# Kernel optimization log

Hardware: AMD Instinct MI355X
Metric: run time of the kernel (lower is better)

Reference implementation:

```python
import jax, jax.numpy as jnp
import numpy as np

B, P, CD, RD, H, NR, OD, T = 1024, 22, 256, 64, 512, 12, 2, 100
IN = OD + 2 + CD + RD  # 324: [pos(2), ball(2), context(256), role_embed(64)]


def setup_inputs() -> dict:
    key = jax.random.key(0)
    ks = jax.random.split(key, 20)
    def n(k, shape, s=1.0):
        return jax.random.normal(k, shape, dtype=jnp.float32) * s
    sH = 1.0 / np.sqrt(H)
    sI = 1.0 / np.sqrt(IN)
    return {
        "context": n(ks[0], (B, P, CD)),
        "initial_position": n(ks[1], (B, P, OD)),
        "ball_landing": n(ks[2], (B, 2)),
        "roles": jax.random.randint(ks[3], (B, P), 0, NR, dtype=jnp.int32),
        "max_steps": T,
        "role_table": n(ks[4], (NR, RD), 0.02),
        # LSTM layer 0 (input_dim=IN)
        "W_ih0": n(ks[5], (4 * H, IN), sI),
        "W_hh0": n(ks[6], (4 * H, H), sH),
        "b0": n(ks[7], (4 * H,), sH),  # b_ih + b_hh fused
        # LSTM layer 1 (input_dim=H)
        "W_ih1": n(ks[8], (4 * H, H), sH),
        "W_hh1": n(ks[9], (4 * H, H), sH),
        "b1": n(ks[10], (4 * H,), sH),
        # output MLP: H -> H//2 -> OD
        "W_fc1": n(ks[11], (H // 2, H), sH),
        "b_fc1": n(ks[12], (H // 2,), sH),
        "W_fc2": n(ks[13], (OD, H // 2), 1.0 / np.sqrt(H // 2)),
        "b_fc2": n(ks[14], (OD,), 0.02),
        # initial_pos_encoder: Linear(OD, H)
        "W_init": n(ks[15], (H, OD), 1.0 / np.sqrt(OD)),
        "b_init": n(ks[16], (H,), 0.02),
    }


def _lstm_cell(x, h, c, W_ih, W_hh, b):
    # PyTorch gate order: i, f, g, o
    gates = x @ W_ih.T + h @ W_hh.T + b  # [N, 4H]
    i, f, g, o = jnp.split(gates, 4, axis=-1)
    c_new = jax.nn.sigmoid(f) * c + jax.nn.sigmoid(i) * jnp.tanh(g)
    h_new = jax.nn.sigmoid(o) * jnp.tanh(c_new)
    return h_new, c_new


def reference(context, initial_position, ball_landing, roles, max_steps,
              role_table, W_ih0, W_hh0, b0, W_ih1, W_hh1, b1,
              W_fc1, b_fc1, W_fc2, b_fc2, W_init, b_init):
    batch, num_players, context_dim = context.shape
    N = batch * num_players
    out_dim = initial_position.shape[-1]

    ctx_flat = context.reshape(N, context_dim)
    role_flat = role_table[roles].reshape(N, -1)
    ball_flat = jnp.broadcast_to(ball_landing[:, None, :], (batch, num_players, 2)).reshape(N, 2)
    static = jnp.concatenate([ball_flat, ctx_flat, role_flat], axis=1)  # [N, IN-2]

    pos0 = initial_position.reshape(N, out_dim)
    h0 = pos0 @ W_init.T + b_init  # initial_pos_encoder into layer-0 hidden
    c0 = jnp.zeros_like(h0)
    h1 = jnp.zeros_like(h0)
    c1 = jnp.zeros_like(h0)

    def step(carry, _):
        pos, h0, c0, h1, c1 = carry
        x = jnp.concatenate([pos, static], axis=1)  # [N, IN]
        h0, c0 = _lstm_cell(x, h0, c0, W_ih0, W_hh0, b0)
        h1, c1 = _lstm_cell(h0, h1, c1, W_ih1, W_hh1, b1)
        # output MLP (dropout inactive in eval)
        nxt = jax.nn.relu(h1 @ W_fc1.T + b_fc1) @ W_fc2.T + b_fc2  # [N, OD]
        return (nxt, h0, c0, h1, c1), nxt

    _, preds = jax.lax.scan(step, (pos0, h0, c0, h1, c1), None, length=max_steps)
    # preds: [T, N, OD] -> [batch, num_players, T, OD]
    preds = preds.transpose(1, 0, 2).reshape(batch, num_players, max_steps, out_dim)
    return preds
```

## Files before the change

### kernel.cpp

```cpp
#include <hip/hip_runtime.h>
#include <cstdint>


#define DEVI __device__ __forceinline__

typedef __bf16 bf16x8 __attribute__((ext_vector_type(8)));
typedef float  f32x4  __attribute__((ext_vector_type(4)));
typedef float  f32x2  __attribute__((ext_vector_type(2)));
typedef unsigned short u16x4 __attribute__((ext_vector_type(4)));

static constexpr int NROWS = 22528;
static constexpr int T_STEPS = 100;
static constexpr int NBM = 176;

DEVI unsigned short f2bf(float f) {
  unsigned u = __float_as_uint(f);
  u = u + 0x7FFFu + ((u >> 16) & 1u);
  return (unsigned short)(u >> 16);
}
DEVI float bf2f(unsigned short h) { return __uint_as_float(((unsigned)h) << 16); }

DEVI float fast_sigmoid(float x) {
  float e = __builtin_amdgcn_exp2f(-1.442695041f * x);
  return __builtin_amdgcn_rcpf(1.0f + e);
}
DEVI float fast_tanh(float x) {
  float e = __builtin_amdgcn_exp2f(2.885390082f * x);
  return 1.0f - 2.0f * __builtin_amdgcn_rcpf(e + 1.0f);
}

DEVI void async_copy16(const void* g, void* l) {
  __builtin_amdgcn_global_load_lds(
      (const __attribute__((address_space(1))) void*)g,
      (__attribute__((address_space(3))) void*)l, 16, 0, 0);
}

template <int KITERS, int KSWITCH>
DEVI void gemm_core(const unsigned short* __restrict__ A1, int lda1,
                    const unsigned short* __restrict__ A2, int lda2,
                    const unsigned short* __restrict__ B1, int ldb1,
                    const unsigned short* __restrict__ B2, int ldb2,
                    unsigned short* lds, f32x4 acc[4][4], int tid) {
  const int lane = tid & 63, wid = tid >> 6;
  const int wm = wid & 1, wn = wid >> 1;
  const int c16 = lane & 15, q = lane >> 4;
#pragma unroll
  for (int i = 0; i < 4; ++i)
#pragma unroll
    for (int j = 0; j < 4; ++j) acc[i][j] = f32x4{0.f, 0.f, 0.f, 0.f};
#pragma unroll
  for (int kt = 0; kt < KITERS; ++kt) {
    const bool sec = (kt >= KSWITCH);
    const unsigned short* Ab = sec ? A2 : A1;
    const unsigned short* Bb = sec ? B2 : B1;
    const int lda = sec ? lda2 : lda1;
    const int ldb = sec ? ldb2 : ldb1;
    const int kk = (sec ? (kt - KSWITCH) : kt) * 64;
    __syncthreads();
#pragma unroll
    for (int rd = 0; rd < 4; ++rd) {
      int p = rd * 256 + tid;
      int row = p >> 3, u = p & 7, ch = u ^ (row & 7);
      async_copy16(Ab + row * lda + kk + ch * 8, lds + p * 8);
      async_copy16(Bb + row * ldb + kk + ch * 8, lds + 8192 + p * 8);
    }
    __syncthreads();
#pragma unroll
    for (int s = 0; s < 2; ++s) {
      bf16x8 a[4], b[4];
#pragma unroll
      for (int mf = 0; mf < 4; ++mf) {
        int row = wm * 64 + mf * 16 + c16;
        int slot = row * 8 + ((s * 4 + q) ^ (row & 7));
        a[mf] = *(const bf16x8*)(lds + slot * 8);
      }
#pragma unroll
      for (int nf = 0; nf < 4; ++nf) {
        int row = wn * 64 + nf * 16 + c16;
        int slot = row * 8 + ((s * 4 + q) ^ (row & 7));
        b[nf] = *(const bf16x8*)(lds + 8192 + slot * 8);
      }
#pragma unroll
      for (int mf = 0; mf < 4; ++mf)
#pragma unroll
        for (int nf = 0; nf < 4; ++nf)
          acc[mf][nf] = __builtin_amdgcn_mfma_f32_16x16x32_bf16(a[mf], b[nf], acc[mf][nf], 0, 0, 0);
    }
  }
}

DEVI int orig_row(int j) {
  int tile = j >> 7, rem = j & 127;
  int half = rem >> 6, g = (rem >> 4) & 3, cc = rem & 15;
  return g * 512 + (tile * 32 + half * 16 + cc);
}

__global__ void k_prep_w(const float* __restrict__ Whh0, const float* __restrict__ Wih1,
                         const float* __restrict__ Whh1, const float* __restrict__ Wih0,
                         const float* __restrict__ Wfc1, const float* __restrict__ b0,
                         const float* __restrict__ b1,
                         unsigned short* __restrict__ W0p, unsigned short* __restrict__ Wc1p,
                         unsigned short* __restrict__ Wsp, unsigned short* __restrict__ Wfc1b,
                         float* __restrict__ Wposx, float* __restrict__ Wposy,
                         float* __restrict__ b0p4, float* __restrict__ b1p4) {
  int j = blockIdx.x;
  int k = threadIdx.x;
  int o = orig_row(j);
  W0p[j * 512 + k]         = f2bf(Whh0[o * 512 + k]);
  Wc1p[j * 1024 + k]       = f2bf(Wih1[o * 512 + k]);
  Wc1p[j * 1024 + 512 + k] = f2bf(Whh1[o * 512 + k]);
  if (k < 384) Wsp[j * 384 + k] = (k < 322) ? f2bf(Wih0[o * 324 + 2 + k]) : (unsigned short)0;
  if (k == 0) {
    int g = (j >> 4) & 3;
    int cg = (j >> 7) * 32 + ((j >> 6) & 1) * 16 + (j & 15);
    Wposx[cg * 4 + g] = Wih0[o * 324 + 0];
    Wposy[cg * 4 + g] = Wih0[o * 324 + 1];
    b0p4[cg * 4 + g] = b0[o];
    b1p4[cg * 4 + g] = b1[o];
  }
  if (j < 256) Wfc1b[j * 512 + k] = f2bf(Wfc1[j * 512 + k]);
}

__global__ void k_init_xs(const float* __restrict__ ball, const float* __restrict__ ctx,
                          const int* __restrict__ roles, const float* __restrict__ role_table,
                          unsigned short* __restrict__ Xs) {
  int n = blockIdx.x, col = threadIdx.x;
  int b = n / 22;
  float v;
  if (col < 2)        v = ball[b * 2 + col];
  else if (col < 258) v = ctx[(size_t)n * 256 + col - 2];
  else if (col < 322) v = role_table[roles[n] * 64 + col - 258];
  else                v = 0.f;
  Xs[(size_t)n * 384 + col] = f2bf(v);
}

__global__ void k_init_state(const float* __restrict__ pos0, const float* __restrict__ Winit,
                             const float* __restrict__ binit, unsigned short* __restrict__ Hcat,
                             float* __restrict__ c0, float* __restrict__ c1,
                             float* __restrict__ posb) {
  int idx = blockIdx.x * 256 + threadIdx.x;
  if (idx >= NROWS * 512) return;
  int n = idx >> 9, c = idx & 511;
  float px = pos0[n * 2 + 0], py = pos0[n * 2 + 1];
  float h0 = binit[c] + Winit[c * 2 + 0] * px + Winit[c * 2 + 1] * py;
  Hcat[(size_t)n * 1024 + c] = f2bf(h0);
  Hcat[(size_t)n * 1024 + 512 + c] = 0;
  c0[idx] = 0.f;
  c1[idx] = 0.f;
  if (c < 2) posb[n * 2 + c] = pos0[n * 2 + c];
}

__global__ __launch_bounds__(256) void k_static(const unsigned short* __restrict__ Xs,
                                                const unsigned short* __restrict__ Wsp,
                                                const float* __restrict__ b0p4,
                                                unsigned short* __restrict__ SP2) {
  __shared__ __align__(16) unsigned short lds[16384];
  int tid = threadIdx.x, bn = blockIdx.x, bm = blockIdx.y;
  f32x4 acc[4][4];
  const unsigned short* Ab = Xs + (size_t)bm * 128 * 384;
  const unsigned short* Bb = Wsp + (size_t)bn * 128 * 384;
  gemm_core<6, 6>(Ab, 384, Ab, 384, Bb, 384, Bb, 384, lds, acc, tid);
  int lane = tid & 63, wid = tid >> 6, wm = wid & 1, wn = wid >> 1;
  int c16 = lane & 15, q = lane >> 4;
  int cg = bn * 32 + wn * 16 + c16;
  f32x4 bb = *(const f32x4*)&b0p4[cg * 4];
#pragma unroll
  for (int mf = 0; mf < 4; ++mf) {
    int row0 = bm * 128 + wm * 64 + mf * 16 + q * 4;
#pragma unroll
    for (int r = 0; r < 4; ++r) {
      u16x4 v;
      v.x = f2bf(acc[mf][0][r] + bb.x);
      v.y = f2bf(acc[mf][1][r] + bb.y);
      v.z = f2bf(acc[mf][2][r] + bb.z);
      v.w = f2bf(acc[mf][3][r] + bb.w);
      ((u16x4*)SP2)[(size_t)(row0 + r) * 512 + cg] = v;
    }
  }
}

DEVI void swz(int l, int& bn, int& bm) {
  int xcd = l & 7, i = l >> 3;
  bn = i & 15;
  bm = xcd + 8 * (i >> 4);
}

template <bool USE_SP>
__global__ __launch_bounds__(256) void k_s1(const unsigned short* __restrict__ cur,
                                            const unsigned short* __restrict__ Xs,
                                            const unsigned short* __restrict__ W0p,
                                            const unsigned short* __restrict__ Wsp,
                                            const unsigned short* __restrict__ SP2,
                                            const float* __restrict__ b0p4,
                                            const float* __restrict__ Wposx,
                                            const float* __restrict__ Wposy,
                                            const float* __restrict__ posb,
                                            float* __restrict__ c0,
                                            unsigned short* __restrict__ nxt) {
  __shared__ __align__(16) unsigned short lds[16384];
  int tid = threadIdx.x, bn, bm;
  swz(blockIdx.x, bn, bm);
  f32x4 acc[4][4];
  const unsigned short* A1 = cur + (size_t)bm * 128 * 1024;
  const unsigned short* B1 = W0p + (size_t)bn * 128 * 512;
  if constexpr (USE_SP) {
    gemm_core<8, 8>(A1, 1024, A1, 1024, B1, 512, B1, 512, lds, acc, tid);
  } else {
    const unsigned short* A2 = Xs + (size_t)bm * 128 * 384;
    const unsigned short* B2 = Wsp + (size_t)bn * 128 * 384;
    gemm_core<14, 8>(A1, 1024, A2, 384, B1, 512, B2, 384, lds, acc, tid);
  }
  int lane = tid & 63, wid = tid >> 6, wm = wid & 1, wn = wid >> 1;
  int c16 = lane & 15, q = lane >> 4;
  int cg = bn * 32 + wn * 16 + c16;
  f32x4 wpx = *(const f32x4*)&Wposx[cg * 4];
  f32x4 wpy = *(const f32x4*)&Wposy[cg * 4];
  f32x4 sb = f32x4{0.f, 0.f, 0.f, 0.f};
  if constexpr (!USE_SP) sb = *(const f32x4*)&b0p4[cg * 4];
#pragma unroll
  for (int mf = 0; mf < 4; ++mf) {
    int row0 = bm * 128 + wm * 64 + mf * 16 + q * 4;
    f32x4 cold = *(const f32x4*)&c0[(size_t)cg * NROWS + row0];
    f32x4 cnew;
#pragma unroll
    for (int r = 0; r < 4; ++r) {
      size_t row = row0 + r;
      f32x2 pv = *(const f32x2*)&posb[row * 2];
      float s0 = sb.x, s1 = sb.y, s2 = sb.z, s3 = sb.w;
      if constexpr (USE_SP) {
        u16x4 sp = ((const u16x4*)SP2)[row * 512 + cg];
        s0 = bf2f(sp.x); s1 = bf2f(sp.y); s2 = bf2f(sp.z); s3 = bf2f(sp.w);
      }
      float gi = acc[mf][0][r] + s0 + pv.x * wpx.x + pv.y * wpy.x;
      float gf = acc[mf][1][r] + s1 + pv.x * wpx.y + pv.y * wpy.y;
      float gg = acc[mf][2][r] + s2 + pv.x * wpx.z + pv.y * wpy.z;
      float go = acc[mf][3][r] + s3 + pv.x * wpx.w + pv.y * wpy.w;
      float cn = fast_sigmoid(gf) * cold[r] + fast_sigmoid(gi) * fast_tanh(gg);
      cnew[r] = cn;
      nxt[row * 1024 + cg] = f2bf(fast_sigmoid(go) * fast_tanh(cn));
    }
    *(f32x4*)&c0[(size_t)cg * NROWS + row0] = cnew;
  }
}

__global__ __launch_bounds__(256) void k_s2(const unsigned short* __restrict__ nxt_in,
                                            const unsigned short* __restrict__ cur,
                                            const unsigned short* __restrict__ Wc1p,
                                            const float* __restrict__ b1p4,
                                            float* __restrict__ c1,
                                            unsigned short* __restrict__ nxt_out) {
  __shared__ __align__(16) unsigned short lds[16384];
  int tid = threadIdx.x, bn, bm;
  swz(blockIdx.x, bn, bm);
  f32x4 acc[4][4];
  const unsigned short* A1 = nxt_in + (size_t)bm * 128 * 1024;
  const unsigned short* A2 = cur + (size_t)bm * 128 * 1024 + 512;
  const unsigned short* B1 = Wc1p + (size_t)bn * 128 * 1024;
  gemm_core<16, 8>(A1, 1024, A2, 1024, B1, 1024, B1 + 512, 1024, lds, acc, tid);
  int lane = tid & 63, wid = tid >> 6, wm = wid & 1, wn = wid >> 1;
  int c16 = lane & 15, q = lane >> 4;
  int cg = bn * 32 + wn * 16 + c16;
  f32x4 bv = *(const f32x4*)&b1p4[cg * 4];
#pragma unroll
  for (int mf = 0; mf < 4; ++mf) {
    int row0 = bm * 128 + wm * 64 + mf * 16 + q * 4;
    f32x4 cold = *(const f32x4*)&c1[(size_t)cg * NROWS + row0];
    f32x4 cnew;
#pragma unroll
    for (int r = 0; r < 4; ++r) {
      size_t row = row0 + r;
      float gi = acc[mf][0][r] + bv.x;
      float gf = acc[mf][1][r] + bv.y;
      float gg = acc[mf][2][r] + bv.z;
      float go = acc[mf][3][r] + bv.w;
      float cn = fast_sigmoid(gf) * cold[r] + fast_sigmoid(gi) * fast_tanh(gg);
      cnew[r] = cn;
      nxt_out[row * 1024 + 512 + cg] = f2bf(fast_sigmoid(go) * fast_tanh(cn));
    }
    *(f32x4*)&c1[(size_t)cg * NROWS + row0] = cnew;
  }
}

__global__ __launch_bounds__(256) void k_s3(const unsigned short* __restrict__ H,
                                            const unsigned short* __restrict__ Wfc1b,
                                            const float* __restrict__ bfc1,
                                            const float* __restrict__ Wfc2,
                                            const float* __restrict__ bfc2,
                                            float* __restrict__ out, float* __restrict__ posb,
                                            int t) {
  __shared__ __align__(16) unsigned short ldsA[32 * 64];
  __shared__ __align__(16) unsigned short ldsB[256 * 64];
  __shared__ float wfc2s[512];
  __shared__ float red[32 * 8];
  int tid = threadIdx.x;
  int l = blockIdx.x, xcd = l & 7, i = l >> 3;
  int b32 = 4 * (xcd + 8 * (i >> 2)) + (i & 3);
  wfc2s[tid] = Wfc2[tid];
  wfc2s[tid + 256] = Wfc2[tid + 256];
  int lane = tid & 63, wid = tid >> 6;
  int c16 = lane & 15, q = lane >> 4;
  f32x4 acc[2][4];
#pragma unroll
  for (int ii = 0; ii < 2; ++ii)
#pragma unroll
    for (int jj = 0; jj < 4; ++jj) acc[ii][jj] = f32x4{0.f, 0.f, 0.f, 0.f};
  const unsigned short* Ab = H + (size_t)b32 * 32 * 1024 + 512;
#pragma unroll
  for (int kt = 0; kt < 8; ++kt) {
    int k0 = kt * 64;
    __syncthreads();
    {
      int p = tid;
      int row = p >> 3, u = p & 7, ch = u ^ (row & 7);
      async_copy16(Ab + row * 1024 + k0 + ch * 8, ldsA + p * 8);
    }
#pragma unroll
    for (int rd = 0; rd < 8; ++rd) {
      int p = rd * 256 + tid;
      int row = p >> 3, u = p & 7, ch = u ^ (row & 7);
      async_copy16(Wfc1b + row * 512 + k0 + ch * 8, ldsB + p * 8);
    }
    __syncthreads();
#pragma unroll
    for (int s = 0; s < 2; ++s) {
      bf16x8 a[2], b[4];
#pragma unroll
      for (int mf = 0; mf < 2; ++mf) {
        int row = mf * 16 + c16;
        int slot = row * 8 + ((s * 4 + q) ^ (row & 7));
        a[mf] = *(const bf16x8*)(ldsA + slot * 8);
      }
#pragma unroll
      for (int nf = 0; nf < 4; ++nf) {
        int row = wid * 64 + nf * 16 + c16;
        int slot = row * 8 + ((s * 4 + q) ^ (row & 7));
        b[nf] = *(const bf16x8*)(ldsB + slot * 8);
      }
#pragma unroll
      for (int mf = 0; mf < 2; ++mf)
#pragma unroll
        for (int nf = 0; nf < 4; ++nf)
          acc[mf][nf] = __builtin_amdgcn_mfma_f32_16x16x32_bf16(a[mf], b[nf], acc[mf][nf], 0, 0, 0);
    }
  }
  float part[2][2][4];
#pragma unroll
  for (int d = 0; d < 2; ++d)
#pragma unroll
    for (int mf = 0; mf < 2; ++mf)
#pragma unroll
      for (int r = 0; r < 4; ++r) part[d][mf][r] = 0.f;
#pragma unroll
  for (int nf = 0; nf < 4; ++nf) {
    int col = wid * 64 + nf * 16 + c16;
    float w0 = wfc2s[col], w1 = wfc2s[256 + col], bv = bfc1[col];
#pragma unroll
    for (int mf = 0; mf < 2; ++mf)
#pragma unroll
      for (int r = 0; r < 4; ++r) {
        float v = acc[mf][nf][r] + bv;
        v = v > 0.f ? v : 0.f;
        part[0][mf][r] += v * w0;
        part[1][mf][r] += v * w1;
      }
  }
#pragma unroll
  for (int st = 1; st < 16; st <<= 1)
#pragma unroll
    for (int d = 0; d < 2; ++d)
#pragma unroll
      for (int mf = 0; mf < 2; ++mf)
#pragma unroll
        for (int r = 0; r < 4; ++r)
          part[d][mf][r] += __shfl_xor(part[d][mf][r], st, 64);
  if (c16 == 0) {
#pragma unroll
    for (int mf = 0; mf < 2; ++mf)
#pragma unroll
      for (int r = 0; r < 4; ++r) {
        int rl = mf * 16 + q * 4 + r;
        red[rl * 8 + wid * 2 + 0] = part[0][mf][r];
        red[rl * 8 + wid * 2 + 1] = part[1][mf][r];
      }
  }
  __syncthreads();
  if (tid < 64) {
    int rl = tid >> 1, d = tid & 1;
    float s = red[rl * 8 + d] + red[rl * 8 + 2 + d] + red[rl * 8 + 4 + d]
            + red[rl * 8 + 6 + d] + bfc2[d];
    int rg = b32 * 32 + rl;
    out[((size_t)rg * T_STEPS + t) * 2 + d] = s;
    posb[rg * 2 + d] = s;
  }
}

extern "C" void kernel_launch(void* const* d_in, const int* in_sizes, int n_in,
                              void* d_out, int out_size, void* d_ws, size_t ws_size,
                              hipStream_t stream) {
  (void)in_sizes; (void)n_in; (void)out_size;
  const float* ctx   = (const float*)d_in[0];
  const float* pos0  = (const float*)d_in[1];
  const float* ball  = (const float*)d_in[2];
  const int*   roles = (const int*)d_in[3];
  const float* role_table = (const float*)d_in[5];
  const float* Wih0 = (const float*)d_in[6];
  const float* Whh0 = (const float*)d_in[7];
  const float* b0   = (const float*)d_in[8];
  const float* Wih1 = (const float*)d_in[9];
  const float* Whh1 = (const float*)d_in[10];
  const float* b1   = (const float*)d_in[11];
  const float* Wfc1 = (const float*)d_in[12];
  const float* bfc1 = (const float*)d_in[13];
  const float* Wfc2 = (const float*)d_in[14];
  const float* bfc2 = (const float*)d_in[15];
  const float* Winit = (const float*)d_in[16];
  const float* binit = (const float*)d_in[17];
  float* out = (float*)d_out;

  char* w = (char*)d_ws;
  size_t used = 0;
  auto alloc = [&](size_t bytes) {
    char* p = w + used;
    used += (bytes + 255) & ~(size_t)255;
    return p;
  };
  unsigned short* W0p   = (unsigned short*)alloc((size_t)2048 * 512 * 2);
  unsigned short* Wc1p  = (unsigned short*)alloc((size_t)2048 * 1024 * 2);
  unsigned short* Wfc1b = (unsigned short*)alloc((size_t)256 * 512 * 2);
  float* Wposx = (float*)alloc(2048 * 4);
  float* Wposy = (float*)alloc(2048 * 4);
  float* b0p4  = (float*)alloc(2048 * 4);
  float* b1p4  = (float*)alloc(2048 * 4);
  float* posb  = (float*)alloc((size_t)NROWS * 2 * 4);
  unsigned short* Hc0 = (unsigned short*)alloc((size_t)NROWS * 1024 * 2);
  float* c0   = (float*)alloc((size_t)NROWS * 512 * 4);
  float* c1   = (float*)alloc((size_t)NROWS * 512 * 4);
  unsigned short* Hc1 = (unsigned short*)alloc((size_t)NROWS * 1024 * 2);

  const size_t SP_BYTES = (size_t)NROWS * 2048 * 2;
  const bool use_sp = (ws_size >= used + SP_BYTES + (1u << 20));

  unsigned short *Xs, *Wsp, *SP2;
  if (use_sp) {
    SP2 = (unsigned short*)alloc(SP_BYTES);
    Xs  = Hc1;
    Wsp = Hc1 + (size_t)NROWS * 384;
  } else {
    SP2 = Hc1;
    Xs  = (unsigned short*)alloc((size_t)NROWS * 384 * 2);
    Wsp = (unsigned short*)alloc((size_t)2048 * 384 * 2);
  }

  k_prep_w<<<2048, 512, 0, stream>>>(Whh0, Wih1, Whh1, Wih0, Wfc1, b0, b1,
                                     W0p, Wc1p, Wsp, Wfc1b, Wposx, Wposy, b0p4, b1p4);
  k_init_xs<<<NROWS, 384, 0, stream>>>(ball, ctx, roles, role_table, Xs);
  k_init_state<<<(NROWS * 512 + 255) / 256, 256, 0, stream>>>(pos0, Winit, binit, Hc0, c0, c1, posb);

  if (use_sp) {
    dim3 gs(16, NBM);
    k_static<<<gs, 256, 0, stream>>>(Xs, Wsp, b0p4, SP2);
  }

  for (int t = 0; t < T_STEPS; ++t) {
    unsigned short* cur = (t & 1) ? Hc1 : Hc0;
    unsigned short* nxt = (t & 1) ? Hc0 : Hc1;
    if (use_sp)
      k_s1<true><<<16 * NBM, 256, 0, stream>>>(cur, Xs, W0p, Wsp, SP2, b0p4, Wposx, Wposy, posb, c0, nxt);
    else
      k_s1<false><<<16 * NBM, 256, 0, stream>>>(cur, Xs, W0p, Wsp, SP2, b0p4, Wposx, Wposy, posb, c0, nxt);
    k_s2<<<16 * NBM, 256, 0, stream>>>(nxt, cur, Wc1p, b1p4, c1, nxt);
    k_s3<<<704, 256, 0, stream>>>(nxt, Wfc1b, bfc1, Wfc2, bfc2, out, posb, t);
  }
}
```

Measured before the change: 22.08 ms.

## Use 256x256 tiles with 8-wave pipelined double-buffered GEMM for LSTM steps

Replaces the 128x128, 4-wave GEMM core in both per-step LSTM kernels with a 256x256 tile, 512-thread kernel. The new kernel uses a deeper asynchronous LDS staging pipeline over four half-K buffers and raises MFMA priority with setprio. The larger tiles halve global and LDS traffic per output and overlap loads with MFMA work. In exchange, each block uses 128KB of LDS and more registers for 8x4 accumulators, and the grid shrinks to 704 blocks, which may limit occupancy and wave balance across CUs.

```diff
diff --git a/kernel.cpp b/kernel.cpp
--- a/kernel.cpp
+++ b/kernel.cpp
@@ -179,47 +179,163 @@
   }
 }
 
-DEVI void swz(int l, int& bn, int& bm) {
-  int xcd = l & 7, i = l >> 3;
-  bn = i & 15;
-  bm = xcd + 8 * (i >> 4);
+
+struct GemmSrc {
+  const unsigned short *A1, *A2, *B1, *B2;
+  int ldA1, ldA2, ldB1, ldB2;
+};
+
+template <int KT, int KSW>
+DEVI void stage_q(const GemmSrc& g, int t, int s, int isB, unsigned short* dst, int tid) {
+  int tt = (t >= KT) ? (t - 2) : t;
+  const bool sec = (tt >= KSW);
+  const unsigned short* base;
+  int ld;
+  if (isB) { base = sec ? g.B2 : g.B1; ld = sec ? g.ldB2 : g.ldB1; }
+  else     { base = sec ? g.A2 : g.A1; ld = sec ? g.ldA2 : g.ldA1; }
+  base += (sec ? (tt - KSW) : tt) * 64 + s * 32;
+#pragma unroll
+  for (int rd = 0; rd < 2; ++rd) {
+    int p = rd * 512 + tid;
+    int row = p >> 2, u = p & 3, ch = u ^ ((row >> 1) & 3);
+    async_copy16(base + row * ld + ch * 8, dst + p * 8);
+  }
+}
+
+#define GBAR   asm volatile("s_barrier" ::: "memory")
+#define VMCNT4 asm volatile("s_waitcnt vmcnt(4)" ::: "memory")
+
+template <int KT, int KSW>
+DEVI void gemm8(const GemmSrc& g, unsigned short* lds, f32x4 acc[8][4], int tid) {
+  const int lane = tid & 63, wid = tid >> 6;
+  const int wm = wid >> 2, wn = wid & 3;
+  const int c16 = lane & 15, q = lane >> 4;
+#pragma unroll
+  for (int i = 0; i < 8; ++i)
+#pragma unroll
+    for (int j = 0; j < 4; ++j) acc[i][j] = f32x4{0.f, 0.f, 0.f, 0.f};
+  unsigned short* A00 = lds;
+  unsigned short* A01 = lds + 8192;
+  unsigned short* B00 = lds + 16384;
+  unsigned short* B01 = lds + 24576;
+  unsigned short* A10 = lds + 32768;
+  unsigned short* A11 = lds + 40960;
+  unsigned short* B10 = lds + 49152;
+  unsigned short* B11 = lds + 57344;
+  const int rowA0 = wm * 128 + c16;
+  const int rowB0 = wn * 64 + c16;
+  stage_q<KT, KSW>(g, 0, 0, 0, A00, tid);
+  stage_q<KT, KSW>(g, 0, 0, 1, B00, tid);
+  stage_q<KT, KSW>(g, 0, 1, 0, A01, tid);
+  stage_q<KT, KSW>(g, 0, 1, 1, B01, tid);
+  stage_q<KT, KSW>(g, 1, 0, 0, A10, tid);
+  stage_q<KT, KSW>(g, 1, 0, 1, B10, tid);
+  VMCNT4;
+  GBAR;
+  bf16x8 a[4], b[4];
+
+#define LOADA(BASE, MG)                                                        \
+  _Pragma("unroll")                                                            \
+  for (int f = 0; f < 4; ++f) {                                                \
+    int row = rowA0 + ((MG) * 4 + f) * 16;                                     \
+    a[f] = *(const bf16x8*)((BASE) + (row * 4 + (q ^ ((row >> 1) & 3))) * 8);  \
+  }
+#define LOADB(BASE)                                                            \
+  _Pragma("unroll")                                                            \
+  for (int f = 0; f < 4; ++f) {                                                \
+    int row = rowB0 + f * 16;                                                  \
+    b[f] = *(const bf16x8*)((BASE) + (row * 4 + (q ^ ((row >> 1) & 3))) * 8);  \
+  }
+#define MFG(MG)                                                                \
+  __builtin_amdgcn_s_setprio(1);                                               \
+  _Pragma("unroll")                                                            \
+  for (int f = 0; f < 4; ++f)                                                  \
+    _Pragma("unroll")                                                          \
+    for (int nf = 0; nf < 4; ++nf)                                             \
+      acc[(MG) * 4 + f][nf] = __builtin_amdgcn_mfma_f32_16x16x32_bf16(         \
+          a[f], b[nf], acc[(MG) * 4 + f][nf], 0, 0, 0);                        \
+  __builtin_amdgcn_s_setprio(0);                                               \
+  __builtin_amdgcn_sched_barrier(0);
+
+#pragma unroll 1
+  for (int it = 0; it < KT / 2; ++it) {
+    const int t0 = 2 * it;
+    LOADA(A00, 0); LOADB(B00);
+    stage_q<KT, KSW>(g, t0 + 1, 1, 0, A11, tid);
+    GBAR; MFG(0); GBAR;
+    LOADA(A00, 1);
+    stage_q<KT, KSW>(g, t0 + 1, 1, 1, B11, tid);
+    GBAR; MFG(1); GBAR;
+    LOADA(A01, 0); LOADB(B01);
+    stage_q<KT, KSW>(g, t0 + 2, 0, 0, A00, tid);
+    GBAR; MFG(0); GBAR;
+    LOADA(A01, 1);
+    stage_q<KT, KSW>(g, t0 + 2, 0, 1, B00, tid);
+    GBAR; MFG(1); VMCNT4; GBAR;
+    LOADA(A10, 0); LOADB(B10);
+    stage_q<KT, KSW>(g, t0 + 2, 1, 0, A01, tid);
+    GBAR; MFG(0); GBAR;
+    LOADA(A10, 1);
+    stage_q<KT, KSW>(g, t0 + 2, 1, 1, B01, tid);
+    GBAR; MFG(1); GBAR;
+    LOADA(A11, 0); LOADB(B11);
+    stage_q<KT, KSW>(g, t0 + 3, 0, 0, A10, tid);
+    GBAR; MFG(0); GBAR;
+    LOADA(A11, 1);
+    stage_q<KT, KSW>(g, t0 + 3, 0, 1, B10, tid);
+    GBAR; MFG(1); VMCNT4; GBAR;
+  }
+  asm volatile("s_waitcnt vmcnt(0)" ::: "memory");
+#undef LOADA
+#undef LOADB
+#undef MFG
+}
+
+DEVI void swz704(int l, int& bn, int& bm) {
+  int xcd = l & 7, ii = l >> 3;
+  bn = ii & 7;
+  bm = (ii >> 3) * 8 + xcd;
 }
 
 template <bool USE_SP>
-__global__ __launch_bounds__(256) void k_s1(const unsigned short* __restrict__ cur,
-                                            const unsigned short* __restrict__ Xs,
-                                            const unsigned short* __restrict__ W0p,
-                                            const unsigned short* __restrict__ Wsp,
-                                            const unsigned short* __restrict__ SP2,
-                                            const float* __restrict__ b0p4,
-                                            const float* __restrict__ Wposx,
-                                            const float* __restrict__ Wposy,
-                                            const float* __restrict__ posb,
-                                            float* __restrict__ c0,
-                                            unsigned short* __restrict__ nxt) {
-  __shared__ __align__(16) unsigned short lds[16384];
-  int tid = threadIdx.x, bn, bm;
-  swz(blockIdx.x, bn, bm);
-  f32x4 acc[4][4];
-  const unsigned short* A1 = cur + (size_t)bm * 128 * 1024;
-  const unsigned short* B1 = W0p + (size_t)bn * 128 * 512;
+__global__ __launch_bounds__(512, 2) void k_s1_8(const unsigned short* __restrict__ cur,
+                                                 const unsigned short* __restrict__ Xs,
+                                                 const unsigned short* __restrict__ W0p,
+                                                 const unsigned short* __restrict__ Wsp,
+                                                 const unsigned short* __restrict__ SP2,
+                                                 const float* __restrict__ b0p4,
+                                                 const float* __restrict__ Wposx,
+                                                 const float* __restrict__ Wposy,
+                                                 const float* __restrict__ posb,
+                                                 float* __restrict__ c0,
+                                                 unsigned short* __restrict__ nxt) {
+  __shared__ __align__(16) unsigned short lds[65536];
+  const int tid = threadIdx.x;
+  int bn, bm;
+  swz704(blockIdx.x, bn, bm);
+  f32x4 acc[8][4];
+  GemmSrc g;
+  g.A1 = cur + (size_t)bm * 256 * 1024; g.ldA1 = 1024;
+  g.B1 = W0p + (size_t)bn * 256 * 512;  g.ldB1 = 512;
   if constexpr (USE_SP) {
-    gemm_core<8, 8>(A1, 1024, A1, 1024, B1, 512, B1, 512, lds, acc, tid);
+    g.A2 = g.A1; g.ldA2 = 1024; g.B2 = g.B1; g.ldB2 = 512;
+    gemm8<8, 8>(g, lds, acc, tid);
   } else {
-    const unsigned short* A2 = Xs + (size_t)bm * 128 * 384;
-    const unsigned short* B2 = Wsp + (size_t)bn * 128 * 384;
-    gemm_core<14, 8>(A1, 1024, A2, 384, B1, 512, B2, 384, lds, acc, tid);
-  }
-  int lane = tid & 63, wid = tid >> 6, wm = wid & 1, wn = wid >> 1;
-  int c16 = lane & 15, q = lane >> 4;
-  int cg = bn * 32 + wn * 16 + c16;
+    g.A2 = Xs + (size_t)bm * 256 * 384;  g.ldA2 = 384;
+    g.B2 = Wsp + (size_t)bn * 256 * 384; g.ldB2 = 384;
+    gemm8<14, 8>(g, lds, acc, tid);
+  }
+  const int lane = tid & 63, wid = tid >> 6;
+  const int wm = wid >> 2, wn = wid & 3;
+  const int c16 = lane & 15, q = lane >> 4;
+  const int cg = bn * 64 + (wn >> 1) * 32 + (wn & 1) * 16 + c16;
   f32x4 wpx = *(const f32x4*)&Wposx[cg * 4];
   f32x4 wpy = *(const f32x4*)&Wposy[cg * 4];
   f32x4 sb = f32x4{0.f, 0.f, 0.f, 0.f};
   if constexpr (!USE_SP) sb = *(const f32x4*)&b0p4[cg * 4];
 #pragma unroll
-  for (int mf = 0; mf < 4; ++mf) {
-    int row0 = bm * 128 + wm * 64 + mf * 16 + q * 4;
+  for (int mf = 0; mf < 8; ++mf) {
+    int row0 = bm * 256 + wm * 128 + mf * 16 + q * 4;
     f32x4 cold = *(const f32x4*)&c0[(size_t)cg * NROWS + row0];
     f32x4 cnew;
 #pragma unroll
@@ -243,27 +359,31 @@
   }
 }
 
-__global__ __launch_bounds__(256) void k_s2(const unsigned short* __restrict__ nxt_in,
-                                            const unsigned short* __restrict__ cur,
-                                            const unsigned short* __restrict__ Wc1p,
-                                            const float* __restrict__ b1p4,
-                                            float* __restrict__ c1,
-                                            unsigned short* __restrict__ nxt_out) {
-  __shared__ __align__(16) unsigned short lds[16384];
-  int tid = threadIdx.x, bn, bm;
-  swz(blockIdx.x, bn, bm);
-  f32x4 acc[4][4];
-  const unsigned short* A1 = nxt_in + (size_t)bm * 128 * 1024;
-  const unsigned short* A2 = cur + (size_t)bm * 128 * 1024 + 512;
-  const unsigned short* B1 = Wc1p + (size_t)bn * 128 * 1024;
-  gemm_core<16, 8>(A1, 1024, A2, 1024, B1, 1024, B1 + 512, 1024, lds, acc, tid);
-  int lane = tid & 63, wid = tid >> 6, wm = wid & 1, wn = wid >> 1;
-  int c16 = lane & 15, q = lane >> 4;
-  int cg = bn * 32 + wn * 16 + c16;
+__global__ __launch_bounds__(512, 2) void k_s2_8(const unsigned short* __restrict__ nxt_in,
+                                                 const unsigned short* __restrict__ cur,
+                                                 const unsigned short* __restrict__ Wc1p,
+                                                 const float* __restrict__ b1p4,
+                                                 float* __restrict__ c1,
+                                                 unsigned short* __restrict__ nxt_out) {
+  __shared__ __align__(16) unsigned short lds[65536];
+  const int tid = threadIdx.x;
+  int bn, bm;
+  swz704(blockIdx.x, bn, bm);
+  f32x4 acc[8][4];
+  GemmSrc g;
+  g.A1 = nxt_in + (size_t)bm * 256 * 1024;      g.ldA1 = 1024;
+  g.A2 = cur + (size_t)bm * 256 * 1024 + 512;   g.ldA2 = 1024;
+  g.B1 = Wc1p + (size_t)bn * 256 * 1024;        g.ldB1 = 1024;
+  g.B2 = g.B1 + 512;                            g.ldB2 = 1024;
+  gemm8<16, 8>(g, lds, acc, tid);
+  const int lane = tid & 63, wid = tid >> 6;
+  const int wm = wid >> 2, wn = wid & 3;
+  const int c16 = lane & 15, q = lane >> 4;
+  const int cg = bn * 64 + (wn >> 1) * 32 + (wn & 1) * 16 + c16;
   f32x4 bv = *(const f32x4*)&b1p4[cg * 4];
 #pragma unroll
-  for (int mf = 0; mf < 4; ++mf) {
-    int row0 = bm * 128 + wm * 64 + mf * 16 + q * 4;
+  for (int mf = 0; mf < 8; ++mf) {
+    int row0 = bm * 256 + wm * 128 + mf * 16 + q * 4;
     f32x4 cold = *(const f32x4*)&c1[(size_t)cg * NROWS + row0];
     f32x4 cnew;
 #pragma unroll
@@ -465,10 +585,12 @@
     unsigned short* cur = (t & 1) ? Hc1 : Hc0;
     unsigned short* nxt = (t & 1) ? Hc0 : Hc1;
     if (use_sp)
-      k_s1<true><<<16 * NBM, 256, 0, stream>>>(cur, Xs, W0p, Wsp, SP2, b0p4, Wposx, Wposy, posb, c0, nxt);
+      k_s1_8<true><<<704, 512, 0, stream>>>(cur, Xs, W0p, Wsp, SP2, b0p4,
+                                            Wposx, Wposy, posb, c0, nxt);
     else
-      k_s1<false><<<16 * NBM, 256, 0, stream>>>(cur, Xs, W0p, Wsp, SP2, b0p4, Wposx, Wposy, posb, c0, nxt);
-    k_s2<<<16 * NBM, 256, 0, stream>>>(nxt, cur, Wc1p, b1p4, c1, nxt);
+      k_s1_8<false><<<704, 512, 0, stream>>>(cur, Xs, W0p, Wsp, SP2, b0p4,
+                                             Wposx, Wposy, posb, c0, nxt);
+    k_s2_8<<<704, 512, 0, stream>>>(nxt, cur, Wc1p, b1p4, c1, nxt);
     k_s3<<<704, 256, 0, stream>>>(nxt, Wfc1b, bfc1, Wfc2, bfc2, out, posb, t);
   }
 }
```

After: 21.78 ms. No clear change (-1.3%).
